# Performance work log

Hardware: AMD Instinct MI355X
Metric: run time of the kernel (lower is better)

The kernel has to match this reference:

```python
import jax, jax.numpy as jnp
import numpy as np

B, L, D = 8, 1024, 1024  # L must equal D for the elementwise sqrt(K) divide to broadcast


def setup_inputs() -> dict:
    key = jax.random.key(0)
    ks = jax.random.split(key, 9)
    # Non-negative inputs/weights/biases so K = x @ Wk.T + bk >= 0 and sqrt(K) is finite.
    rc = jax.random.uniform(ks[0], (B, L, D), dtype=jnp.float32)
    ri = jax.random.uniform(ks[1], (B, L, D), dtype=jnp.float32)
    tc = jax.random.uniform(ks[2], (B, L, D), dtype=jnp.float32)
    scale = 0.02
    Wq = jax.random.uniform(ks[3], (D, D), dtype=jnp.float32) * scale
    Wk = jax.random.uniform(ks[4], (D, D), dtype=jnp.float32) * scale
    Wv = jax.random.uniform(ks[5], (D, D), dtype=jnp.float32) * scale
    bq = jax.random.uniform(ks[6], (D,), dtype=jnp.float32) * scale
    bk = jax.random.uniform(ks[7], (D,), dtype=jnp.float32) * scale
    bv = jax.random.uniform(ks[8], (D,), dtype=jnp.float32) * scale
    return {
        "reference_caption": rc,
        "reference_image": ri,
        "target_caption": tc,
        "Wq": Wq, "bq": bq,
        "Wk": Wk, "bk": bk,
        "Wv": Wv, "bv": bv,
    }


def reference(reference_caption, reference_image, target_caption, Wq, bq, Wk, bk, Wv, bv):
    # torch nn.Linear: y = x @ W.T + b
    Q = reference_caption @ Wq.T + bq          # [B, Lq, D]
    K = reference_image @ Wk.T + bk            # [B, Lk, D]
    V = reference_image @ Wv.T + bv            # [B, Lk, D]
    matmul_qk = jnp.einsum("bqd,bkd->bqk", Q, K)  # [B, Lq, Lk]
    # Faithful to source: elementwise divide by sqrt(K) tensor (broadcasts since Lq==Lk==D).
    scaled_logits = matmul_qk / jnp.sqrt(K)
    attention_weights = jax.nn.softmax(scaled_logits, axis=-1)
    output = jnp.einsum("bqk,bkd->bqd", attention_weights, V)
    return (output, attention_weights)
```

## Files before the change

### kernel.cpp

```cpp
#include <hip/hip_runtime.h>
#include <hip/hip_fp16.h>
#include <math.h>

typedef unsigned short u16;
typedef __attribute__((ext_vector_type(8))) _Float16 half8;
typedef __attribute__((ext_vector_type(4))) float f32x4;

#define ASLOT 4096
#define SLOT  12288

__device__ __forceinline__ u16 f2h(float f){ __half h=__float2half(f); u16 r; __builtin_memcpy(&r,&h,2); return r; }
__device__ __forceinline__ float h2f(u16 u){ __half h; __builtin_memcpy(&h,&u,2); return __half2float(h); }

#define SYNC1 do{ __builtin_amdgcn_sched_barrier(0); __builtin_amdgcn_s_barrier(); \
    asm volatile("s_waitcnt lgkmcnt(0)" ::: "memory"); __builtin_amdgcn_sched_barrier(0); \
    __builtin_amdgcn_s_setprio(1); }while(0)
#define SYNC2 do{ __builtin_amdgcn_s_setprio(0); __builtin_amdgcn_sched_barrier(0); \
    __builtin_amdgcn_s_barrier(); }while(0)

template<int EPI, int BIASM>
__device__ __forceinline__ void gemm8(
    const u16* __restrict__ A, const u16* __restrict__ B,
    const float* __restrict__ bias,
    float* __restrict__ of, u16* __restrict__ oh,
    const float* __restrict__ cm, u16* __restrict__ od,
    int by, int bx, int lda, int ldb, int ldc, int K, u16* sh)
{
    const int tid  = threadIdx.x;
    const int lane = tid & 63, wv = tid >> 6;
    const int wr = (wv >> 2) * 128;
    const int wc = (wv & 3) * 64;
    const int row0 = by * 256, col0 = bx * 256;
    const int lr = lane & 15, hi = lane >> 4;

    f32x4 acc[8][4];
#pragma unroll
    for (int m = 0; m < 8; m++)
#pragma unroll
        for (int n = 0; n < 4; n++) acc[m][n] = (f32x4){0.f, 0.f, 0.f, 0.f};

    auto STG = [&](int op, int kt, int half){
        const u16* G = op ? B : A;
        const int  ld = op ? ldb : lda;
        const int  rb = (op ? col0 : row0) + half * 128;
        const int  k0 = kt << 6;
        u16* dst = sh + ((kt & 1) << 15) + (op << 14) + (half << 13);
#pragma unroll
        for (int p = 0; p < 2; ++p){
            const int lin = tid + p * 512;
            const int r   = lin >> 3;
            const int cg  = (lin & 7) ^ (r & 7);
            const u16* g = G + (size_t)(rb + r) * ld + k0 + cg * 8;
            __builtin_amdgcn_global_load_lds(
                (__attribute__((address_space(1))) void*)g,
                (__attribute__((address_space(3))) void*)(dst + (size_t)lin * 8), 16, 0, 0);
        }
    };
    auto LDA_ = [&](half8* a, int kt, int mh){
        const u16* base = sh + ((kt & 1) << 15) + ((wr >> 7) << 13);
#pragma unroll
        for (int mi = 0; mi < 4; ++mi)
#pragma unroll
            for (int ks = 0; ks < 2; ++ks){
                const int row = (mh * 4 + mi) * 16 + lr;
                a[mi * 2 + ks] = *(const half8*)&base[row * 64 + (((hi + ks * 4) ^ (lr & 7)) * 8)];
            }
    };
    auto LDB_ = [&](half8* b, int kt, int nh){
        const u16* base = sh + ((kt & 1) << 15) + 16384 + ((wc >> 7) << 13);
        const int wcl = wc & 127;
#pragma unroll
        for (int ni = 0; ni < 2; ++ni)
#pragma unroll
            for (int ks = 0; ks < 2; ++ks){
                const int row = wcl + (nh * 2 + ni) * 16 + lr;
                b[ni * 2 + ks] = *(const half8*)&base[row * 64 + (((hi + ks * 4) ^ (lr & 7)) * 8)];
            }
    };
    auto MM = [&](half8* a, half8* b, int mh, int nh){
#pragma unroll
        for (int mi = 0; mi < 4; ++mi)
#pragma unroll
            for (int ni = 0; ni < 2; ++ni)
#pragma unroll
                for (int ks = 0; ks < 2; ++ks)
                    acc[mh * 4 + mi][nh * 2 + ni] = __builtin_amdgcn_mfma_f32_16x16x32_f16(
                        a[mi * 2 + ks], b[ni * 2 + ks], acc[mh * 4 + mi][nh * 2 + ni], 0, 0, 0);
    };

    const int NKT = K >> 6, NIT = NKT >> 1;
    STG(0, 0, 0); STG(0, 0, 1); STG(1, 0, 0); STG(1, 0, 1);
    STG(1, 1, 0); STG(1, 1, 1); STG(0, 1, 0);
    asm volatile("s_waitcnt vmcnt(6)" ::: "memory");
    __builtin_amdgcn_s_barrier();

    half8 a[8], b0[4], b1[4];
    for (int i = 0; i < NIT; ++i){
        const int t0 = 2 * i, t1 = 2 * i + 1;
        const bool m0 = (t0 + 2 < NKT), m1 = (t1 + 2 < NKT);
        LDA_(a, t0, 0); LDB_(b0, t0, 0);
        STG(0, t1, 1);
        SYNC1; MM(a, b0, 0, 0); SYNC2;
        LDB_(b1, t0, 1);
        SYNC1; MM(a, b1, 0, 1); SYNC2;
        LDA_(a, t0, 1);
        if (m0) STG(1, t0 + 2, 0);
        SYNC1; MM(a, b1, 1, 1); SYNC2;
        if (m0) { STG(1, t0 + 2, 1); STG(0, t0 + 2, 0); }
        if (m0) asm volatile("s_waitcnt vmcnt(6)" ::: "memory");
        else    asm volatile("s_waitcnt vmcnt(0)" ::: "memory");
        SYNC1; MM(a, b0, 1, 0); SYNC2;
        LDA_(a, t1, 0); LDB_(b0, t1, 0);
        if (m0) STG(0, t0 + 2, 1);
        SYNC1; MM(a, b0, 0, 0); SYNC2;
        LDB_(b1, t1, 1);
        SYNC1; MM(a, b1, 0, 1); SYNC2;
        LDA_(a, t1, 1);
        if (m1) STG(1, t1 + 2, 0);
        SYNC1; MM(a, b1, 1, 1); SYNC2;
        if (m1) { STG(1, t1 + 2, 1); STG(0, t1 + 2, 0); }
        if (m1) asm volatile("s_waitcnt vmcnt(6)" ::: "memory");
        else    asm volatile("s_waitcnt vmcnt(0)" ::: "memory");
        SYNC1; MM(a, b0, 1, 0); SYNC2;
    }

#pragma unroll
    for (int m = 0; m < 8; m++){
        const int rb = row0 + wr + m * 16 + hi * 4;
#pragma unroll
        for (int n = 0; n < 4; n++){
            const int c = col0 + wc + n * 16 + lr;
            const float bc = (BIASM == 1) ? bias[c] : 0.f;
#pragma unroll
            for (int q = 0; q < 4; q++){
                const int r = rb + q;
                float v = acc[m][n][q] + bc;
                if (BIASM == 2) v += bias[r];
                const size_t idx = (size_t)r * ldc + c;
                if (EPI == 0) of[idx] = v;
                else if (EPI == 1) oh[idx] = f2h(v);
                else {
                    const float d  = v - cm[(size_t)((r >> 10) << 10) + c];
                    const u16  dh = f2h(d);
                    oh[idx] = dh;
                    od[idx] = f2h(d - h2f(dh));
                }
            }
        }
    }
}

__global__ __launch_bounds__(512, 1) void lin_qk_k(
    const u16* __restrict__ rc_h, const u16* __restrict__ ri_h,
    const u16* __restrict__ Wq_h, const u16* __restrict__ Wk_h,
    const float* __restrict__ bq, const float* __restrict__ bk,
    const float* __restrict__ cm,
    u16* __restrict__ Q_h, u16* __restrict__ Kd, u16* __restrict__ Krs)
{
    __shared__ __align__(16) u16 sh[65536];
    const int nwg = gridDim.x, chunk = nwg >> 3;
    const int swz = ((int)blockIdx.x & 7) * chunk + ((int)blockIdx.x >> 3);
    const int p = swz & 1, t = swz >> 1;
    if (p == 0) {
        gemm8<1, 1>(rc_h, Wq_h, bq, nullptr, Q_h, nullptr, nullptr,
                    t >> 2, t & 3, 1024, 1024, 1024, 1024, sh);
    } else {
        gemm8<5, 1>(ri_h, Wk_h, bk, nullptr, Kd, cm, Krs,
                    t >> 2, t & 3, 1024, 1024, 1024, 1024, sh);
    }
}

__global__ __launch_bounds__(512, 1) void qkt_vt_k(
    const u16* __restrict__ Q_h, const u16* __restrict__ Kd,
    const u16* __restrict__ ri_h, const u16* __restrict__ Wv_h,
    const float* __restrict__ bv, const float* __restrict__ u,
    float* __restrict__ wts, u16* __restrict__ Vt)
{
    __shared__ __align__(16) u16 sh[65536];
    const int nwg = gridDim.x, chunk = nwg >> 3;
    const int swz = ((int)blockIdx.x & 7) * chunk + ((int)blockIdx.x >> 3);
    const int p = swz & 1, t = swz >> 1;
    if (p == 0) {
        const int z = t >> 4, rem = t & 15;
        gemm8<0, 2>(Q_h + ((size_t)z << 20), Kd + ((size_t)z << 20),
                    u + ((size_t)z << 10), wts + ((size_t)z << 20), nullptr,
                    nullptr, nullptr,
                    rem >> 2, rem & 3, 1024, 1024, 1024, 1024, sh);
    } else {
        gemm8<1, 2>(Wv_h, ri_h, bv, nullptr, Vt, nullptr, nullptr,
                    t >> 5, t & 31, 1024, 1024, 8192, 1024, sh);
    }
}

__device__ __forceinline__ void stage_tile2(const u16* __restrict__ G, int rowbase, int ldg,
                                            int k0, u16* Ls, int tid, int rows){
    for (int p = 0; p < rows / 64; ++p){
        const int lin = tid + p * 256;
        const int row = lin >> 2;
        const int cg  = ((lin & 3) ^ ((row >> 1) & 3)) * 8;
        const u16* g = G + (size_t)(rowbase + row) * ldg + (k0 + cg);
        __builtin_amdgcn_global_load_lds(
            (__attribute__((address_space(1))) void*)g,
            (__attribute__((address_space(3))) void*)(Ls + (size_t)lin * 8), 16, 0, 0);
    }
}

__device__ __forceinline__ void gemm_core2(
    const u16* __restrict__ A, const u16* __restrict__ B,
    float* __restrict__ of,
    int by, int bx, int lda, int ldb, int ldc, int K, u16* sh)
{
    const int tid  = threadIdx.x;
    const int lane = tid & 63, wv = tid >> 6;
    const int wr = (wv >> 1) * 64;
    const int wc = (wv & 1) * 128;
    const int row0 = by * 128, col0 = bx * 256;
    const int lr = lane & 15, hi = lane >> 4;
    const int co = (hi ^ ((lr >> 1) & 3)) * 8;

    f32x4 acc[4][8];
#pragma unroll
    for (int m = 0; m < 4; m++)
#pragma unroll
        for (int n = 0; n < 8; n++) acc[m][n] = (f32x4){0.f, 0.f, 0.f, 0.f};

    auto stage_set = [&](int buf, int k0){
        u16* s = sh + buf * SLOT;
        stage_tile2(A, row0, lda, k0, s, tid, 128);
        stage_tile2(B, col0, ldb, k0, s + ASLOT, tid, 256);
    };

    const int NIT = K >> 5;
    stage_set(0, 0);
    stage_set(1, 32);
    int bufs = 2, bufr = 0;
    for (int t = 0; t < NIT; ++t){
        if (t + 2 < NIT){ stage_set(bufs, (t + 2) << 5); bufs = (bufs + 1 == 3) ? 0 : bufs + 1; }
        const int rem = NIT - 1 - t;
        if (rem >= 2)      asm volatile("s_waitcnt vmcnt(12)" ::: "memory");
        else if (rem == 1) asm volatile("s_waitcnt vmcnt(6)" ::: "memory");
        else               asm volatile("s_waitcnt vmcnt(0)" ::: "memory");
        __builtin_amdgcn_s_barrier();
        __builtin_amdgcn_sched_barrier(0);

        const u16* s = sh + bufr * SLOT;
        bufr = (bufr + 1 == 3) ? 0 : bufr + 1;

        half8 a[4], b[8];
#pragma unroll
        for (int m = 0; m < 4; m++) a[m] = *(const half8*)&s[(wr + m * 16 + lr) * 32 + co];
#pragma unroll
        for (int n = 0; n < 8; n++) b[n] = *(const half8*)&s[ASLOT + (wc + n * 16 + lr) * 32 + co];
#pragma unroll
        for (int m = 0; m < 4; m++)
#pragma unroll
            for (int n = 0; n < 8; n++)
                acc[m][n] = __builtin_amdgcn_mfma_f32_16x16x32_f16(a[m], b[n], acc[m][n], 0, 0, 0);
        __builtin_amdgcn_sched_barrier(0);
        __builtin_amdgcn_s_barrier();
    }

#pragma unroll
    for (int m = 0; m < 4; m++) {
        const int rb = row0 + wr + m * 16 + hi * 4;
#pragma unroll
        for (int n = 0; n < 8; n++) {
            const int c = col0 + wc + n * 16 + lr;
#pragma unroll
            for (int q = 0; q < 4; q++)
                of[(size_t)(rb + q) * ldc + c] = acc[m][n][q];
        }
    }
}

__global__ __launch_bounds__(256, 2) void av_k(
    const u16* __restrict__ W_h, const u16* __restrict__ Vt, float* __restrict__ outp)
{
    __shared__ __align__(16) u16 sh[3 * SLOT];
    const int nwg = gridDim.x, chunk = nwg >> 3;
    const int wg = ((int)blockIdx.x & 7) * chunk + ((int)blockIdx.x >> 3);
    const int z = wg >> 5, rem = wg & 31;
    gemm_core2(W_h + ((size_t)z << 20), Vt + (size_t)z * 1024,
               outp + ((size_t)z << 20),
               rem >> 2, rem & 3, 1024, 8192, 1024, 1024, sh);
}

__global__ __launch_bounds__(256)
void colmean_k(const u16* __restrict__ ri_h, float* __restrict__ xbar)
{
    const int b = blockIdx.x >> 5, sub = blockIdx.x & 31;
    const int dg = sub & 3, rg = sub >> 2;
    const int d = dg * 256 + threadIdx.x;
    const u16* base = ri_h + ((size_t)b << 20) + ((size_t)(rg * 128) << 10) + d;
    float s = 0.f;
#pragma unroll 4
    for (int r = 0; r < 128; ++r) s += h2f(base[(size_t)r << 10]);
    atomicAdd(&xbar[(b << 10) + d], s * (1.f / 1024.f));
}

template<bool BIAS, bool AFULL>
__global__ __launch_bounds__(256)
void rowdot_k(const u16* __restrict__ A, const float* __restrict__ B,
              const float* __restrict__ bias, float* __restrict__ out)
{
    const int o = blockIdx.x * 4 + (threadIdx.x >> 6);
    const int lane = threadIdx.x & 63;
    const int ar = AFULL ? o : (o & 1023);
    const int br = o >> 10;
    const u16* ap = A + ((size_t)ar << 10);
    const float* bp = B + ((size_t)br << 10);
    float s = 0.f;
#pragma unroll
    for (int j = 0; j < 16; ++j){ const int i = lane + (j << 6); s += h2f(ap[i]) * bp[i]; }
#pragma unroll
    for (int off = 32; off >= 1; off >>= 1) s += __shfl_xor(s, off);
    if (lane == 0) out[o] = s + (BIAS ? bias[ar] : 0.f);
}

__global__ __launch_bounds__(256)
void softmax_scale_k(float* __restrict__ W, const u16* __restrict__ Kd,
                     const u16* __restrict__ Krs, const float* __restrict__ cm,
                     u16* __restrict__ Wh)
{
    const long row = blockIdx.x;
    const int b = (int)(row >> 10);
    float* p = W + (row << 10);
    const int tid = threadIdx.x;

    float4 v = ((const float4*)p)[tid];
    const ushort4 kd = ((const ushort4*)(Kd + (row << 10)))[tid];
    const ushort4 ks = ((const ushort4*)(Krs + (row << 10)))[tid];
    const float4 cmv = ((const float4*)(cm + ((size_t)b << 10)))[tid];
    v.x *= rsqrtf(h2f(kd.x) + h2f(ks.x) + cmv.x);
    v.y *= rsqrtf(h2f(kd.y) + h2f(ks.y) + cmv.y);
    v.z *= rsqrtf(h2f(kd.z) + h2f(ks.z) + cmv.z);
    v.w *= rsqrtf(h2f(kd.w) + h2f(ks.w) + cmv.w);

    float m = fmaxf(fmaxf(v.x, v.y), fmaxf(v.z, v.w));
#pragma unroll
    for (int o = 32; o >= 1; o >>= 1) m = fmaxf(m, __shfl_xor(m, o));
    __shared__ float sm[4];
    const int wid = tid >> 6, lane = tid & 63;
    if (lane == 0) sm[wid] = m;
    __syncthreads();
    m = fmaxf(fmaxf(sm[0], sm[1]), fmaxf(sm[2], sm[3]));

    v.x = __expf(v.x - m); v.y = __expf(v.y - m);
    v.z = __expf(v.z - m); v.w = __expf(v.w - m);
    float s = v.x + v.y + v.z + v.w;
#pragma unroll
    for (int o = 32; o >= 1; o >>= 1) s += __shfl_xor(s, o);
    __shared__ float ss[4];
    if (lane == 0) ss[wid] = s;
    __syncthreads();
    s = ss[0] + ss[1] + ss[2] + ss[3];

    const float inv = 1.0f / s;
    v.x *= inv; v.y *= inv; v.z *= inv; v.w *= inv;
    ((float4*)p)[tid] = v;

    ushort4 ub;
    ub.x = f2h(v.x); ub.y = f2h(v.y); ub.z = f2h(v.z); ub.w = f2h(v.w);
    ((ushort4*)(Wh + (row << 10)))[tid] = ub;
}

__global__ __launch_bounds__(256)
void conv_plain5_k(const float4* __restrict__ x0, ushort4* __restrict__ y0,
                   const float4* __restrict__ x1, ushort4* __restrict__ y1,
                   const float4* __restrict__ x2, ushort4* __restrict__ y2,
                   const float4* __restrict__ x3, ushort4* __restrict__ y3,
                   const float4* __restrict__ x4, ushort4* __restrict__ y4)
{
    const long i = (long)blockIdx.x * 256 + threadIdx.x;
    const long n0 = 2097152, n1 = 262144;
    const float4* x; ushort4* y; long j;
    if (i < n0)                 { x = x0; y = y0; j = i; }
    else if (i < 2*n0)          { x = x1; y = y1; j = i - n0; }
    else if (i < 2*n0 + n1)     { x = x2; y = y2; j = i - 2*n0; }
    else if (i < 2*n0 + 2*n1)   { x = x3; y = y3; j = i - 2*n0 - n1; }
    else                        { x = x4; y = y4; j = i - 2*n0 - 2*n1; }
    const float4 v = x[j];
    ushort4 o;
    o.x = f2h(v.x); o.y = f2h(v.y); o.z = f2h(v.z); o.w = f2h(v.w);
    y[j] = o;
}

extern "C" void kernel_launch(void* const* d_in, const int* in_sizes, int n_in,
                              void* d_out, int out_size, void* d_ws, size_t ws_size,
                              hipStream_t stream)
{
    const float* rc = (const float*)d_in[0];
    const float* ri = (const float*)d_in[1];
    const float* Wq = (const float*)d_in[3];
    const float* bq = (const float*)d_in[4];
    const float* Wk = (const float*)d_in[5];
    const float* bk = (const float*)d_in[6];
    const float* Wv = (const float*)d_in[7];
    const float* bv = (const float*)d_in[8];

    const long M8 = 8192 * 1024L;
    const long M1 = 1024 * 1024L;

    u16* ws   = (u16*)d_ws;
    u16* ri_h = ws;
    u16* rc_h = ws + 1 * M8;
    u16* Kd   = ws + 2 * M8;
    u16* Krs  = ws + 3 * M8;
    u16* Wq_h = ws + 4 * M8;
    u16* Wk_h = Wq_h + M1;
    u16* Wv_h = Wk_h + M1;
    float* xbar = (float*)(ws + 4 * M8 + 3 * M1);
    float* cm   = xbar + 8192;
    float* uu   = cm + 8192;

    float* outp = (float*)d_out;
    float* wts  = outp + M8;
    u16*   Q_h  = (u16*)d_out;
    u16*   Vt   = rc_h;
    u16*   W_h  = ri_h;

    conv_plain5_k<<<19456, 256, 0, stream>>>(
        (const float4*)ri, (ushort4*)ri_h, (const float4*)rc, (ushort4*)rc_h,
        (const float4*)Wq, (ushort4*)Wq_h, (const float4*)Wk, (ushort4*)Wk_h,
        (const float4*)Wv, (ushort4*)Wv_h);

    hipMemsetAsync(xbar, 0, 8192 * sizeof(float), stream);
    colmean_k<<<256, 256, 0, stream>>>(ri_h, xbar);
    rowdot_k<true, false><<<2048, 256, 0, stream>>>(Wk_h, xbar, bk, cm);

    lin_qk_k<<<256, 512, 0, stream>>>(rc_h, ri_h, Wq_h, Wk_h, bq, bk, cm, Q_h, Kd, Krs);

    rowdot_k<false, true><<<2048, 256, 0, stream>>>(Q_h, cm, nullptr, uu);

    qkt_vt_k<<<256, 512, 0, stream>>>(Q_h, Kd, ri_h, Wv_h, bv, uu, wts, Vt);

    softmax_scale_k<<<8192, 256, 0, stream>>>(wts, Kd, Krs, cm, W_h);

    av_k<<<256, 256, 0, stream>>>(W_h, Vt, outp);
}
```

Baseline: 158.4 us.

## Fuse sqrt(K) scaling into QK^T epilogue and retile Q/K projection GEMM

```diff
diff --git a/kernel.cpp b/kernel.cpp
--- a/kernel.cpp
+++ b/kernel.cpp
@@ -17,6 +17,107 @@
     __builtin_amdgcn_s_setprio(1); }while(0)
 #define SYNC2 do{ __builtin_amdgcn_s_setprio(0); __builtin_amdgcn_sched_barrier(0); \
     __builtin_amdgcn_s_barrier(); }while(0)
+
+template<int ROWS>
+__device__ __forceinline__ void stage_tile2(const u16* __restrict__ G, int rowbase, int ldg,
+                                            int k0, u16* Ls, int tid){
+#pragma unroll
+    for (int p = 0; p < ROWS / 64; ++p){
+        const int lin = tid + p * 256;
+        const int row = lin >> 2;
+        const int cg  = ((lin & 3) ^ ((row >> 1) & 3)) * 8;
+        const u16* g = G + (size_t)(rowbase + row) * ldg + (k0 + cg);
+        __builtin_amdgcn_global_load_lds(
+            (__attribute__((address_space(1))) void*)g,
+            (__attribute__((address_space(3))) void*)(Ls + (size_t)lin * 8), 16, 0, 0);
+    }
+}
+
+template<int EPI, int BIASM>
+__device__ __forceinline__ void gemm_core(
+    const u16* __restrict__ A, const u16* __restrict__ B,
+    const float* __restrict__ bias,
+    float* __restrict__ of, u16* __restrict__ oh,
+    const float* __restrict__ cm, u16* __restrict__ od,
+    int by, int bx, int lda, int ldb, int ldc, int K, u16* sh)
+{
+    const int tid  = threadIdx.x;
+    const int lane = tid & 63, wv = tid >> 6;
+    const int wr = (wv >> 1) * 64;
+    const int wc = (wv & 1) * 128;
+    const int row0 = by * 128, col0 = bx * 256;
+    const int lr = lane & 15, hi = lane >> 4;
+    const int co = (hi ^ ((lr >> 1) & 3)) * 8;
+
+    f32x4 acc[4][8];
+#pragma unroll
+    for (int m = 0; m < 4; m++)
+#pragma unroll
+        for (int n = 0; n < 8; n++) acc[m][n] = (f32x4){0.f, 0.f, 0.f, 0.f};
+
+    auto stage_set = [&](int buf, int k0){
+        u16* s = sh + buf * SLOT;
+        stage_tile2<128>(A, row0, lda, k0, s, tid);
+        stage_tile2<256>(B, col0, ldb, k0, s + ASLOT, tid);
+    };
+
+    const int NIT = K >> 5;
+    stage_set(0, 0);
+    stage_set(1, 32);
+    int bufs = 2, bufr = 0;
+    for (int t = 0; t < NIT; ++t){
+        if (t + 2 < NIT){ stage_set(bufs, (t + 2) << 5); bufs = (bufs + 1 == 3) ? 0 : bufs + 1; }
+        const int rem = NIT - 1 - t;
+        if (rem >= 2)      asm volatile("s_waitcnt vmcnt(12)" ::: "memory");
+        else if (rem == 1) asm volatile("s_waitcnt vmcnt(6)" ::: "memory");
+        else               asm volatile("s_waitcnt vmcnt(0)" ::: "memory");
+        __builtin_amdgcn_s_barrier();
+        __builtin_amdgcn_sched_barrier(0);
+
+        const u16* s = sh + bufr * SLOT;
+        bufr = (bufr + 1 == 3) ? 0 : bufr + 1;
+
+        half8 a[4], b[8];
+#pragma unroll
+        for (int m = 0; m < 4; m++) a[m] = *(const half8*)&s[(wr + m * 16 + lr) * 32 + co];
+#pragma unroll
+        for (int n = 0; n < 8; n++) b[n] = *(const half8*)&s[ASLOT + (wc + n * 16 + lr) * 32 + co];
+#pragma unroll
+        for (int m = 0; m < 4; m++)
+#pragma unroll
+            for (int n = 0; n < 8; n++)
+                acc[m][n] = __builtin_amdgcn_mfma_f32_16x16x32_f16(a[m], b[n], acc[m][n], 0, 0, 0);
+        __builtin_amdgcn_sched_barrier(0);
+        __builtin_amdgcn_s_barrier();
+    }
+
+    const int bbase = (row0 >> 10) << 10;
+#pragma unroll
+    for (int m = 0; m < 4; m++) {
+        const int rb = row0 + wr + m * 16 + hi * 4;
+#pragma unroll
+        for (int n = 0; n < 8; n++) {
+            const int c = col0 + wc + n * 16 + lr;
+            const float bc = (BIASM == 1) ? bias[c] : 0.f;
+            const float cmn = (EPI == 5) ? cm[bbase + c] : 0.f;
+#pragma unroll
+            for (int q = 0; q < 4; q++) {
+                const int r = rb + q;
+                float v = acc[m][n][q] + bc;
+                if (BIASM == 2) v += bias[r];
+                const size_t idx = (size_t)r * ldc + c;
+                if (EPI == 0) of[idx] = v;
+                else if (EPI == 1) oh[idx] = f2h(v);
+                else {
+                    const float d  = v - cmn;
+                    const u16  dh = f2h(d);
+                    oh[idx] = dh;
+                    od[idx] = f2h(d - h2f(dh));
+                }
+            }
+        }
+    }
+}
 
 template<int EPI, int BIASM>
 __device__ __forceinline__ void gemm8(
@@ -131,49 +232,49 @@
         for (int n = 0; n < 4; n++){
             const int c = col0 + wc + n * 16 + lr;
             const float bc = (BIASM == 1) ? bias[c] : 0.f;
+            const float cmn = (EPI == 6) ? cm[c] : 0.f;
 #pragma unroll
             for (int q = 0; q < 4; q++){
                 const int r = rb + q;
                 float v = acc[m][n][q] + bc;
                 if (BIASM == 2) v += bias[r];
                 const size_t idx = (size_t)r * ldc + c;
-                if (EPI == 0) of[idx] = v;
-                else if (EPI == 1) oh[idx] = f2h(v);
+                if (EPI == 1) oh[idx] = f2h(v);
                 else {
-                    const float d  = v - cm[(size_t)((r >> 10) << 10) + c];
-                    const u16  dh = f2h(d);
-                    oh[idx] = dh;
-                    od[idx] = f2h(d - h2f(dh));
+                    const float kk = h2f(oh[idx]) + h2f(od[idx]) + cmn;
+                    of[idx] = v * rsqrtf(kk);
                 }
             }
         }
     }
 }
 
-__global__ __launch_bounds__(512, 1) void lin_qk_k(
+__global__ __launch_bounds__(256, 2) void lin_qk_k(
     const u16* __restrict__ rc_h, const u16* __restrict__ ri_h,
     const u16* __restrict__ Wq_h, const u16* __restrict__ Wk_h,
     const float* __restrict__ bq, const float* __restrict__ bk,
     const float* __restrict__ cm,
     u16* __restrict__ Q_h, u16* __restrict__ Kd, u16* __restrict__ Krs)
 {
-    __shared__ __align__(16) u16 sh[65536];
+    __shared__ __align__(16) u16 sh[3 * SLOT];
     const int nwg = gridDim.x, chunk = nwg >> 3;
     const int swz = ((int)blockIdx.x & 7) * chunk + ((int)blockIdx.x >> 3);
     const int p = swz & 1, t = swz >> 1;
     if (p == 0) {
-        gemm8<1, 1>(rc_h, Wq_h, bq, nullptr, Q_h, nullptr, nullptr,
-                    t >> 2, t & 3, 1024, 1024, 1024, 1024, sh);
+        gemm_core<1, 1>(rc_h, Wq_h, bq, nullptr, Q_h, nullptr, nullptr,
+                        t >> 2, t & 3, 1024, 1024, 1024, 1024, sh);
     } else {
-        gemm8<5, 1>(ri_h, Wk_h, bk, nullptr, Kd, cm, Krs,
-                    t >> 2, t & 3, 1024, 1024, 1024, 1024, sh);
+        gemm_core<5, 1>(ri_h, Wk_h, bk, nullptr, Kd, cm, Krs,
+                        t >> 2, t & 3, 1024, 1024, 1024, 1024, sh);
     }
 }
 
 __global__ __launch_bounds__(512, 1) void qkt_vt_k(
     const u16* __restrict__ Q_h, const u16* __restrict__ Kd,
+    const u16* __restrict__ Krs,
     const u16* __restrict__ ri_h, const u16* __restrict__ Wv_h,
     const float* __restrict__ bv, const float* __restrict__ u,
+    const float* __restrict__ cm,
     float* __restrict__ wts, u16* __restrict__ Vt)
 {
     __shared__ __align__(16) u16 sh[65536];
@@ -182,9 +283,10 @@
     const int p = swz & 1, t = swz >> 1;
     if (p == 0) {
         const int z = t >> 4, rem = t & 15;
-        gemm8<0, 2>(Q_h + ((size_t)z << 20), Kd + ((size_t)z << 20),
-                    u + ((size_t)z << 10), wts + ((size_t)z << 20), nullptr,
-                    nullptr, nullptr,
+        gemm8<6, 2>(Q_h + ((size_t)z << 20), Kd + ((size_t)z << 20),
+                    u + ((size_t)z << 10), wts + ((size_t)z << 20),
+                    (u16*)(Kd + ((size_t)z << 20)), cm + ((size_t)z << 10),
+                    (u16*)(Krs + ((size_t)z << 20)),
                     rem >> 2, rem & 3, 1024, 1024, 1024, 1024, sh);
     } else {
         gemm8<1, 2>(Wv_h, ri_h, bv, nullptr, Vt, nullptr, nullptr,
@@ -192,87 +294,6 @@
     }
 }
 
-__device__ __forceinline__ void stage_tile2(const u16* __restrict__ G, int rowbase, int ldg,
-                                            int k0, u16* Ls, int tid, int rows){
-    for (int p = 0; p < rows / 64; ++p){
-        const int lin = tid + p * 256;
-        const int row = lin >> 2;
-        const int cg  = ((lin & 3) ^ ((row >> 1) & 3)) * 8;
-        const u16* g = G + (size_t)(rowbase + row) * ldg + (k0 + cg);
-        __builtin_amdgcn_global_load_lds(
-            (__attribute__((address_space(1))) void*)g,
-            (__attribute__((address_space(3))) void*)(Ls + (size_t)lin * 8), 16, 0, 0);
-    }
-}
-
-__device__ __forceinline__ void gemm_core2(
-    const u16* __restrict__ A, const u16* __restrict__ B,
-    float* __restrict__ of,
-    int by, int bx, int lda, int ldb, int ldc, int K, u16* sh)
-{
-    const int tid  = threadIdx.x;
-    const int lane = tid & 63, wv = tid >> 6;
-    const int wr = (wv >> 1) * 64;
-    const int wc = (wv & 1) * 128;
-    const int row0 = by * 128, col0 = bx * 256;
-    const int lr = lane & 15, hi = lane >> 4;
-    const int co = (hi ^ ((lr >> 1) & 3)) * 8;
-
-    f32x4 acc[4][8];
-#pragma unroll
-    for (int m = 0; m < 4; m++)
-#pragma unroll
-        for (int n = 0; n < 8; n++) acc[m][n] = (f32x4){0.f, 0.f, 0.f, 0.f};
-
-    auto stage_set = [&](int buf, int k0){
-        u16* s = sh + buf * SLOT;
-        stage_tile2(A, row0, lda, k0, s, tid, 128);
-        stage_tile2(B, col0, ldb, k0, s + ASLOT, tid, 256);
-    };
-
-    const int NIT = K >> 5;
-    stage_set(0, 0);
-    stage_set(1, 32);
-    int bufs = 2, bufr = 0;
-    for (int t = 0; t < NIT; ++t){
-        if (t + 2 < NIT){ stage_set(bufs, (t + 2) << 5); bufs = (bufs + 1 == 3) ? 0 : bufs + 1; }
-        const int rem = NIT - 1 - t;
-        if (rem >= 2)      asm volatile("s_waitcnt vmcnt(12)" ::: "memory");
-        else if (rem == 1) asm volatile("s_waitcnt vmcnt(6)" ::: "memory");
-        else               asm volatile("s_waitcnt vmcnt(0)" ::: "memory");
-        __builtin_amdgcn_s_barrier();
-        __builtin_amdgcn_sched_barrier(0);
-
-        const u16* s = sh + bufr * SLOT;
-        bufr = (bufr + 1 == 3) ? 0 : bufr + 1;
-
-        half8 a[4], b[8];
-#pragma unroll
-        for (int m = 0; m < 4; m++) a[m] = *(const half8*)&s[(wr + m * 16 + lr) * 32 + co];
-#pragma unroll
-        for (int n = 0; n < 8; n++) b[n] = *(const half8*)&s[ASLOT + (wc + n * 16 + lr) * 32 + co];
-#pragma unroll
-        for (int m = 0; m < 4; m++)
-#pragma unroll
-            for (int n = 0; n < 8; n++)
-                acc[m][n] = __builtin_amdgcn_mfma_f32_16x16x32_f16(a[m], b[n], acc[m][n], 0, 0, 0);
-        __builtin_amdgcn_sched_barrier(0);
-        __builtin_amdgcn_s_barrier();
-    }
-
-#pragma unroll
-    for (int m = 0; m < 4; m++) {
-        const int rb = row0 + wr + m * 16 + hi * 4;
-#pragma unroll
-        for (int n = 0; n < 8; n++) {
-            const int c = col0 + wc + n * 16 + lr;
-#pragma unroll
-            for (int q = 0; q < 4; q++)
-                of[(size_t)(rb + q) * ldc + c] = acc[m][n][q];
-        }
-    }
-}
-
 __global__ __launch_bounds__(256, 2) void av_k(
     const u16* __restrict__ W_h, const u16* __restrict__ Vt, float* __restrict__ outp)
 {
@@ -280,9 +301,9 @@
     const int nwg = gridDim.x, chunk = nwg >> 3;
     const int wg = ((int)blockIdx.x & 7) * chunk + ((int)blockIdx.x >> 3);
     const int z = wg >> 5, rem = wg & 31;
-    gemm_core2(W_h + ((size_t)z << 20), Vt + (size_t)z * 1024,
-               outp + ((size_t)z << 20),
-               rem >> 2, rem & 3, 1024, 8192, 1024, 1024, sh);
+    gemm_core<0, 0>(W_h + ((size_t)z << 20), Vt + (size_t)z * 1024,
+                    nullptr, outp + ((size_t)z << 20), nullptr, nullptr, nullptr,
+                    rem >> 2, rem & 3, 1024, 8192, 1024, 1024, sh);
 }
 
 __global__ __launch_bounds__(256)
@@ -318,24 +339,13 @@
 }
 
 __global__ __launch_bounds__(256)
-void softmax_scale_k(float* __restrict__ W, const u16* __restrict__ Kd,
-                     const u16* __restrict__ Krs, const float* __restrict__ cm,
-                     u16* __restrict__ Wh)
+void softmax_k(float* __restrict__ W, u16* __restrict__ Wh)
 {
     const long row = blockIdx.x;
-    const int b = (int)(row >> 10);
     float* p = W + (row << 10);
     const int tid = threadIdx.x;
 
     float4 v = ((const float4*)p)[tid];
-    const ushort4 kd = ((const ushort4*)(Kd + (row << 10)))[tid];
-    const ushort4 ks = ((const ushort4*)(Krs + (row << 10)))[tid];
-    const float4 cmv = ((const float4*)(cm + ((size_t)b << 10)))[tid];
-    v.x *= rsqrtf(h2f(kd.x) + h2f(ks.x) + cmv.x);
-    v.y *= rsqrtf(h2f(kd.y) + h2f(ks.y) + cmv.y);
-    v.z *= rsqrtf(h2f(kd.z) + h2f(ks.z) + cmv.z);
-    v.w *= rsqrtf(h2f(kd.w) + h2f(ks.w) + cmv.w);
-
     float m = fmaxf(fmaxf(v.x, v.y), fmaxf(v.z, v.w));
 #pragma unroll
     for (int o = 32; o >= 1; o >>= 1) m = fmaxf(m, __shfl_xor(m, o));
@@ -428,13 +438,13 @@
     colmean_k<<<256, 256, 0, stream>>>(ri_h, xbar);
     rowdot_k<true, false><<<2048, 256, 0, stream>>>(Wk_h, xbar, bk, cm);
 
-    lin_qk_k<<<256, 512, 0, stream>>>(rc_h, ri_h, Wq_h, Wk_h, bq, bk, cm, Q_h, Kd, Krs);
+    lin_qk_k<<<512, 256, 0, stream>>>(rc_h, ri_h, Wq_h, Wk_h, bq, bk, cm, Q_h, Kd, Krs);
 
     rowdot_k<false, true><<<2048, 256, 0, stream>>>(Q_h, cm, nullptr, uu);
 
-    qkt_vt_k<<<256, 512, 0, stream>>>(Q_h, Kd, ri_h, Wv_h, bv, uu, wts, Vt);
-
-    softmax_scale_k<<<8192, 256, 0, stream>>>(wts, Kd, Krs, cm, W_h);
+    qkt_vt_k<<<256, 512, 0, stream>>>(Q_h, Kd, Krs, ri_h, Wv_h, bv, uu, cm, wts, Vt);
+
+    softmax_k<<<8192, 256, 0, stream>>>(wts, W_h);
 
     av_k<<<256, 256, 0, stream>>>(W_h, Vt, outp);
 }
```

Measured after the change: 160.7 us. No clear change (+1.4%).
